# Performance work log

Measured on AMD Instinct MI355X. Metric: run time of the kernel, lower is better.

The kernel has to match this reference:

```python
import jax, jax.numpy as jnp
import numpy as np

NEG_SLOPE_GAT = 0.2   # GATConv internal leaky_relu slope (PyG default)
NEG_SLOPE = 0.01      # nn.LeakyReLU default slope


def _gat(h_src_in, h_dst_in, src, dst, Wsrc, Wdst, a_s, a_d, b, n_dst, self_loops):
    """Single-head PyG-style GATConv: gather -> score -> edge softmax -> scatter-sum."""
    hs = h_src_in @ Wsrc            # [N_src, C]
    hd = h_dst_in @ Wdst            # [N_dst, C]
    if self_loops:                  # static flag; same node set on both sides
        loop = jnp.arange(n_dst, dtype=src.dtype)
        src = jnp.concatenate([src, loop])
        dst = jnp.concatenate([dst, loop])
    # attention logits per edge
    e = jax.nn.leaky_relu((hs @ a_s)[src] + (hd @ a_d)[dst], NEG_SLOPE_GAT)  # [E]
    # softmax over edges sharing a destination node
    m = jax.ops.segment_max(e, dst, num_segments=n_dst)
    ex = jnp.exp(e - m[dst])
    denom = jax.ops.segment_sum(ex, dst, num_segments=n_dst)
    alpha = ex / denom[dst]
    out = jax.ops.segment_sum(hs[src] * alpha[:, None], dst, num_segments=n_dst)
    return out + b


def setup_inputs() -> dict:
    key = jax.random.key(0)
    ks = iter(jax.random.split(key, 64))
    NB, NP = 100_000, 50_000
    E_bb, E_pp, E_bp = 800_000, 400_000, 400_000
    FB, FP, H, H2 = 32, 34, 64, 32
    rn = lambda shape, s=0.05: jax.random.normal(next(ks), shape, jnp.float32) * s
    d = {}
    d['x_b'] = rn((NB, FB), 1.0)
    d['x_p'] = rn((NP, FP), 1.0)
    d['ei_bb'] = jax.random.randint(next(ks), (2, E_bb), 0, NB, jnp.int32)
    d['ei_pp'] = jax.random.randint(next(ks), (2, E_pp), 0, NP, jnp.int32)
    d['ei_bp_src'] = jax.random.randint(next(ks), (E_bp,), 0, NB, jnp.int32)
    d['ei_bp_dst'] = jax.random.randint(next(ks), (E_bp,), 0, NP, jnp.int32)
    d['W_in_b'] = rn((FB, H)); d['b_in_b'] = jnp.zeros((H,), jnp.float32)
    d['W_in_p'] = rn((FP, H)); d['b_in_p'] = jnp.zeros((H,), jnp.float32)
    for tag, cin, cout in (('1', H, H), ('2', H, H2)):
        d['W_bb' + tag] = rn((cin, cout)); d['as_bb' + tag] = rn((cout,)); d['ad_bb' + tag] = rn((cout,)); d['b_bb' + tag] = jnp.zeros((cout,), jnp.float32)
        d['W_pp' + tag] = rn((cin, cout)); d['as_pp' + tag] = rn((cout,)); d['ad_pp' + tag] = rn((cout,)); d['b_pp' + tag] = jnp.zeros((cout,), jnp.float32)
        d['Ws_bp' + tag] = rn((cin, cout)); d['Wd_bp' + tag] = rn((cin, cout)); d['as_bp' + tag] = rn((cout,)); d['ad_bp' + tag] = rn((cout,)); d['b_bp' + tag] = jnp.zeros((cout,), jnp.float32)
    d['W_out'] = rn((H2, 1)); d['b_out'] = jnp.zeros((1,), jnp.float32)
    return d


def reference(x_b, x_p, ei_bb, ei_pp, ei_bp_src, ei_bp_dst,
              W_in_b, b_in_b, W_in_p, b_in_p,
              W_bb1, as_bb1, ad_bb1, b_bb1, W_pp1, as_pp1, ad_pp1, b_pp1,
              Ws_bp1, Wd_bp1, as_bp1, ad_bp1, b_bp1,
              W_bb2, as_bb2, ad_bb2, b_bb2, W_pp2, as_pp2, ad_pp2, b_pp2,
              Ws_bp2, Wd_bp2, as_bp2, ad_bp2, b_bp2,
              W_out, b_out):
    NB, NP = x_b.shape[0], x_p.shape[0]
    lr = lambda v: jax.nn.leaky_relu(v, NEG_SLOPE)
    # input projections (dropout is eval-mode identity)
    hb = lr(x_b @ W_in_b + b_in_b)
    hp = lr(x_p @ W_in_p + b_in_p)
    # hetero conv 1 (sum aggregation over relations sharing a dst type)
    ob = _gat(hb, hb, ei_bb[0], ei_bb[1], W_bb1, W_bb1, as_bb1, ad_bb1, b_bb1, NB, True)
    op = (_gat(hp, hp, ei_pp[0], ei_pp[1], W_pp1, W_pp1, as_pp1, ad_pp1, b_pp1, NP, True)
          + _gat(hb, hp, ei_bp_src, ei_bp_dst, Ws_bp1, Wd_bp1, as_bp1, ad_bp1, b_bp1, NP, False))
    hb, hp = lr(ob), lr(op)
    # hetero conv 2
    ob2 = _gat(hb, hb, ei_bb[0], ei_bb[1], W_bb2, W_bb2, as_bb2, ad_bb2, b_bb2, NB, True)
    op2 = (_gat(hp, hp, ei_pp[0], ei_pp[1], W_pp2, W_pp2, as_pp2, ad_pp2, b_pp2, NP, True)
           + _gat(hb, hp, ei_bp_src, ei_bp_dst, Ws_bp2, Wd_bp2, as_bp2, ad_bp2, b_bp2, NP, False))
    hp = lr(op2)
    return hp @ W_out + b_out  # [NP, 1]
```

## Files before the change

### kernel.cpp

```cpp
#include <hip/hip_runtime.h>
#include <hip/hip_bf16.h>
#include <cstdint>
#include <cstddef>


typedef __attribute__((ext_vector_type(8))) short short8;
typedef __attribute__((ext_vector_type(4))) float f32x4;

#define ABITS 10
#define CHUNKE 8192

static __device__ __forceinline__ float b2f(__hip_bfloat16 v) { return __bfloat162float(v); }

static __device__ __forceinline__ float ldf(const void* p, int i, int bf) {
    return bf ? __bfloat162float(((const __hip_bfloat16*)p)[i]) : ((const float*)p)[i];
}

static __device__ __forceinline__ short f2bs(float f) {
    __hip_bfloat16 h = __float2bfloat16(f);
    return *reinterpret_cast<short*>(&h);
}
static __device__ __forceinline__ float bs2f(short s) {
    __hip_bfloat16 h = *reinterpret_cast<__hip_bfloat16*>(&s);
    return __bfloat162float(h);
}
static __device__ __forceinline__ float sel4(const float* a, int i) {
    return i == 0 ? a[0] : i == 1 ? a[1] : i == 2 ? a[2] : a[3];
}
static __device__ __forceinline__ float lrelu2(float x) { return x > 0.f ? x : 0.2f * x; }

__global__ __launch_bounds__(256) void k_detect(const unsigned* __restrict__ w,
                                                int* __restrict__ flag)
{
    __shared__ int s_cnt;
    if (threadIdx.x == 0) s_cnt = 0;
    __syncthreads();
    int c = 0;
#pragma unroll
    for (int j = 0; j < 4; ++j) {
        unsigned u = w[threadIdx.x * 4 + j];
        unsigned e = (u >> 7) & 0xffu;
        c += (e >= 100u && e <= 145u) ? 1 : 0;
    }
    atomicAdd(&s_cnt, c);
    __syncthreads();
    if (threadIdx.x == 0) *flag = (s_cnt > 614) ? 1 : 0;
}


__global__ __launch_bounds__(256) void k_bkt_hist(
    const int* __restrict__ bb_d, const int* __restrict__ pp_d,
    const int* __restrict__ bp_d, int* __restrict__ histM,
    int E_bb, int E_pp, int E_bp, int NB, int NP, int nbkt, int nblk)
{
    __shared__ int h[256];
    for (int i = threadIdx.x; i < nbkt; i += 256) h[i] = 0;
    __syncthreads();
    int E_all = E_bb + E_pp + E_bp;
    int base = blockIdx.x * CHUNKE;
    int end = base + CHUNKE < E_all ? base + CHUNKE : E_all;
    for (int i = base + threadIdx.x; i < end; i += 256) {
        int d;
        if (i < E_bb) d = bb_d[i];
        else if (i < E_bb + E_pp) d = NB + pp_d[i - E_bb];
        else d = NB + NP + bp_d[i - E_bb - E_pp];
        atomicAdd(&h[d >> ABITS], 1);
    }
    __syncthreads();
    for (int i = threadIdx.x; i < nbkt; i += 256)
        histM[(size_t)i * nblk + blockIdx.x] = h[i];
}

__global__ __launch_bounds__(1024) void k_scan1(const int* __restrict__ deg,
                                                int* __restrict__ out,
                                                int* __restrict__ bsum, int n)
{
    __shared__ int wsum[16];
    int gid = blockIdx.x * 1024 + threadIdx.x;
    int lane = threadIdx.x & 63, wid = threadIdx.x >> 6;
    int v = (gid < n) ? deg[gid] : 0;
    int x = v;
#pragma unroll
    for (int off = 1; off < 64; off <<= 1) {
        int y = __shfl_up(x, off, 64);
        if (lane >= off) x += y;
    }
    if (lane == 63) wsum[wid] = x;
    __syncthreads();
    if (wid == 0 && lane < 16) {
        int w0 = wsum[lane];
#pragma unroll
        for (int off = 1; off < 16; off <<= 1) {
            int y = __shfl_up(w0, off, 16);
            if (lane >= off) w0 += y;
        }
        wsum[lane] = w0;
    }
    __syncthreads();
    int base = (wid > 0) ? wsum[wid - 1] : 0;
    int incl = base + x;
    if (gid < n) out[gid] = incl - v;
    if (threadIdx.x == 1023) bsum[blockIdx.x] = incl;
}

__global__ __launch_bounds__(1024) void k_scan2(int* __restrict__ bsum, int nb)
{
    __shared__ int wsum[16];
    int lane = threadIdx.x & 63, wid = threadIdx.x >> 6;
    int v = (threadIdx.x < nb) ? bsum[threadIdx.x] : 0;
    int x = v;
#pragma unroll
    for (int off = 1; off < 64; off <<= 1) {
        int y = __shfl_up(x, off, 64);
        if (lane >= off) x += y;
    }
    if (lane == 63) wsum[wid] = x;
    __syncthreads();
    if (wid == 0 && lane < 16) {
        int w0 = wsum[lane];
#pragma unroll
        for (int off = 1; off < 16; off <<= 1) {
            int y = __shfl_up(w0, off, 16);
            if (lane >= off) w0 += y;
        }
        wsum[lane] = w0;
    }
    __syncthreads();
    int base = (wid > 0) ? wsum[wid - 1] : 0;
    if (threadIdx.x < nb) bsum[threadIdx.x] = base + x - v;
}

__global__ __launch_bounds__(1024) void k_scan3(int* __restrict__ indptr,
                                                const int* __restrict__ bsum,
                                                int n, int E)
{
    int gid = blockIdx.x * 1024 + threadIdx.x;
    if (gid < n) indptr[gid] += bsum[blockIdx.x];
    if (gid == 0) indptr[n] = E;
}

__global__ __launch_bounds__(256) void k_bkt_scatter(
    const int* __restrict__ bb_s, const int* __restrict__ bb_d,
    const int* __restrict__ pp_s, const int* __restrict__ pp_d,
    const int* __restrict__ bp_s, const int* __restrict__ bp_d,
    const int* __restrict__ histS, unsigned* __restrict__ ebuf,
    int E_bb, int E_pp, int E_bp, int NB, int NP, int nbkt, int nblk)
{
    __shared__ int cur[256];
    for (int i = threadIdx.x; i < nbkt; i += 256)
        cur[i] = histS[(size_t)i * nblk + blockIdx.x];
    __syncthreads();
    int E_all = E_bb + E_pp + E_bp;
    int base = blockIdx.x * CHUNKE;
    int end = base + CHUNKE < E_all ? base + CHUNKE : E_all;
    for (int i = base + threadIdx.x; i < end; i += 256) {
        int s, d;
        if (i < E_bb) { s = bb_s[i]; d = bb_d[i]; }
        else if (i < E_bb + E_pp) { int j = i - E_bb; s = pp_s[j]; d = NB + pp_d[j]; }
        else { int j = i - E_bb - E_pp; s = bp_s[j]; d = NB + NP + bp_d[j]; }
        int p = atomicAdd(&cur[d >> ABITS], 1);
        ebuf[p] = ((unsigned)(d & ((1 << ABITS) - 1)) << 20) | (unsigned)s;
    }
}

__global__ __launch_bounds__(256) void k_deg(
    const unsigned* __restrict__ ebuf, const int* __restrict__ histS,
    int* __restrict__ deg, int NALL, int E_all, int nbkt, int nblk)
{
    __shared__ int h[1 << ABITS];
    int b = blockIdx.x;
    int d0 = b << ABITS;
    int nloc = NALL - d0 < (1 << ABITS) ? NALL - d0 : (1 << ABITS);
    for (int i = threadIdx.x; i < nloc; i += 256) h[i] = 0;
    __syncthreads();
    int s0 = histS[(size_t)b * nblk];
    int s1 = histS[(size_t)(b + 1) * nblk];
    for (int i = s0 + threadIdx.x; i < s1; i += 256)
        atomicAdd(&h[ebuf[i] >> 20], 1);
    __syncthreads();
    for (int i = threadIdx.x; i < nloc; i += 256) deg[d0 + i] = h[i];
}

__global__ __launch_bounds__(256) void k_place(
    const unsigned* __restrict__ ebuf, const int* __restrict__ histS,
    const int* __restrict__ ip, int* __restrict__ sidx,
    int NALL, int E_all, int nbkt, int nblk)
{
    __shared__ int cur[1 << ABITS];
    int b = blockIdx.x;
    int d0 = b << ABITS;
    int nloc = NALL - d0 < (1 << ABITS) ? NALL - d0 : (1 << ABITS);
    for (int i = threadIdx.x; i < nloc; i += 256) cur[i] = ip[d0 + i];
    __syncthreads();
    int s0 = histS[(size_t)b * nblk];
    int s1 = histS[(size_t)(b + 1) * nblk];
    for (int i = s0 + threadIdx.x; i < s1; i += 256) {
        unsigned e = ebuf[i];
        int p = atomicAdd(&cur[e >> 20], 1);
        sidx[p] = (int)(e & 0xFFFFFu);
    }
}

template <int CIN>
__global__ __launch_bounds__(256) void k_in_proj_mfma(
    const void* __restrict__ X, const void* __restrict__ W, const void* __restrict__ B,
    __hip_bfloat16* __restrict__ Y, int M, const int* __restrict__ flag)
{
    const int bf = *flag;
    constexpr int KP = 40;
    __shared__ short WT[64 * KP];
    __shared__ float bl[64];
    for (int i = threadIdx.x; i < CIN * 64; i += 256) {
        int k = i / 64, n = i % 64;
        WT[n * KP + k] = f2bs(ldf(W, i, bf));
    }
    if (threadIdx.x < 64) bl[threadIdx.x] = ldf(B, threadIdx.x, bf);
    __syncthreads();

    int lane = threadIdx.x & 63;
    int wv   = threadIdx.x >> 6;
    int m = lane & 15, quad = lane >> 4;
    int row0 = (blockIdx.x * 4 + wv) * 16;
    if (row0 >= M) return;

    int arow = row0 + m; if (arow >= M) arow = M - 1;
    short8 a;
#pragma unroll
    for (int j = 0; j < 8; ++j)
        a[j] = f2bs(ldf(X, arow * CIN + quad * 8 + j, bf));

    f32x4 acc[4] = {};
#pragma unroll
    for (int t = 0; t < 4; ++t) {
        short8 b = *(const short8*)&WT[((lane & 15) + 16 * t) * KP + quad * 8];
        acc[t] = __builtin_amdgcn_mfma_f32_16x16x32_bf16(a, b, acc[t], 0, 0, 0);
    }

    if (CIN == 34) {
        float x32[4], x33[4];
#pragma unroll
        for (int r = 0; r < 4; ++r) {
            int row = row0 + quad * 4 + r; if (row >= M) row = M - 1;
            x32[r] = ldf(X, row * CIN + 32, bf);
            x33[r] = ldf(X, row * CIN + 33, bf);
        }
#pragma unroll
        for (int t = 0; t < 4; ++t) {
            int col = (lane & 15) + 16 * t;
            float w32 = bs2f(WT[col * KP + 32]);
            float w33 = bs2f(WT[col * KP + 33]);
#pragma unroll
            for (int r = 0; r < 4; ++r)
                acc[t][r] += x32[r] * w32 + x33[r] * w33;
        }
    }

#pragma unroll
    for (int t = 0; t < 4; ++t) {
        int col = (lane & 15) + 16 * t;
        float bb = bl[col];
#pragma unroll
        for (int r = 0; r < 4; ++r) {
            int row = row0 + quad * 4 + r;
            if (row < M) {
                float v = acc[t][r] + bb;
                v = v > 0.f ? v : 0.01f * v;
                Y[(size_t)row * 64 + col] = __float2bfloat16(v);
            }
        }
    }
}

template <int N, bool STORE>
__global__ __launch_bounds__(256) void k_gat_proj_mfma(
    const __hip_bfloat16* __restrict__ H, const void* __restrict__ W,
    const void* __restrict__ a_s, const void* __restrict__ a_d,
    __hip_bfloat16* __restrict__ HS, float* __restrict__ SS, float* __restrict__ SD,
    int M, const int* __restrict__ flag)
{
    const int bf = *flag;
    constexpr int KP = 72;
    constexpr int T = N / 16;
    __shared__ short WT[N * KP];
    for (int i = threadIdx.x; i < 64 * N; i += 256) {
        int k = i / N, n = i % N;
        WT[n * KP + k] = f2bs(ldf(W, i, bf));
    }
    __syncthreads();

    int lane = threadIdx.x & 63;
    int wv   = threadIdx.x >> 6;
    int m = lane & 15, quad = lane >> 4;
    int row0 = (blockIdx.x * 4 + wv) * 16;
    if (row0 >= M) return;

    const short* Hs = (const short*)H;
    int arow = row0 + m; if (arow >= M) arow = M - 1;

    f32x4 acc[T] = {};
#pragma unroll
    for (int ks = 0; ks < 2; ++ks) {
        short8 a = *(const short8*)&Hs[(size_t)arow * 64 + ks * 32 + quad * 8];
#pragma unroll
        for (int t = 0; t < T; ++t) {
            short8 b = *(const short8*)&WT[((lane & 15) + 16 * t) * KP + ks * 32 + quad * 8];
            acc[t] = __builtin_amdgcn_mfma_f32_16x16x32_bf16(a, b, acc[t], 0, 0, 0);
        }
    }

    float asv[T], adv[T];
#pragma unroll
    for (int t = 0; t < T; ++t) {
        int col = (lane & 15) + 16 * t;
        asv[t] = ldf(a_s, col, bf);
        adv[t] = ldf(a_d, col, bf);
    }
    float vs[4] = {}, vd[4] = {};
#pragma unroll
    for (int t = 0; t < T; ++t)
#pragma unroll
        for (int r = 0; r < 4; ++r) {
            vs[r] += acc[t][r] * asv[t];
            vd[r] += acc[t][r] * adv[t];
        }
#pragma unroll
    for (int off = 1; off < 16; off <<= 1)
#pragma unroll
        for (int r = 0; r < 4; ++r) {
            vs[r] += __shfl_xor(vs[r], off);
            vd[r] += __shfl_xor(vd[r], off);
        }
    int c = lane & 15;
    if (c < 8) {
        int row = row0 + quad * 4 + (c & 3);
        if (row < M) {
            if (c < 4) SS[row] = sel4(vs, c & 3);
            else       SD[row] = sel4(vd, c & 3);
        }
    }

    if (STORE) {
#pragma unroll
        for (int t = 0; t < T; ++t) {
            int col = (lane & 15) + 16 * t;
#pragma unroll
            for (int r = 0; r < 4; ++r) {
                int row = row0 + quad * 4 + r;
                if (row < M)
                    HS[(size_t)row * N + col] = __float2bfloat16(acc[t][r]);
            }
        }
    }
}

template <int N1, int N2, bool S1, bool S2>
__global__ __launch_bounds__(256) void k_gat_proj_dual(
    const __hip_bfloat16* __restrict__ H,
    const void* __restrict__ W1, const void* __restrict__ W2,
    const void* __restrict__ as1, const void* __restrict__ ad1,
    const void* __restrict__ as2, const void* __restrict__ ad2,
    __hip_bfloat16* __restrict__ HS1, __hip_bfloat16* __restrict__ HS2,
    float* __restrict__ SS1, float* __restrict__ SD1,
    float* __restrict__ SS2, float* __restrict__ SD2,
    int M, const int* __restrict__ flag)
{
    const int bf = *flag;
    constexpr int KP = 72;
    constexpr int T1 = N1 / 16, T2 = N2 / 16, T = T1 + T2;
    __shared__ short WT[(N1 + N2) * KP];
    for (int i = threadIdx.x; i < 64 * N1; i += 256) {
        int k = i / N1, n = i % N1;
        WT[n * KP + k] = f2bs(ldf(W1, i, bf));
    }
    for (int i = threadIdx.x; i < 64 * N2; i += 256) {
        int k = i / N2, n = i % N2;
        WT[(N1 + n) * KP + k] = f2bs(ldf(W2, i, bf));
    }
    __syncthreads();

    int lane = threadIdx.x & 63;
    int wv   = threadIdx.x >> 6;
    int m = lane & 15, quad = lane >> 4;
    int row0 = (blockIdx.x * 4 + wv) * 16;
    if (row0 >= M) return;

    const short* Hs = (const short*)H;
    int arow = row0 + m; if (arow >= M) arow = M - 1;

    f32x4 acc[T] = {};
#pragma unroll
    for (int ks = 0; ks < 2; ++ks) {
        short8 a = *(const short8*)&Hs[(size_t)arow * 64 + ks * 32 + quad * 8];
#pragma unroll
        for (int t = 0; t < T; ++t) {
            short8 b = *(const short8*)&WT[((lane & 15) + 16 * t) * KP + ks * 32 + quad * 8];
            acc[t] = __builtin_amdgcn_mfma_f32_16x16x32_bf16(a, b, acc[t], 0, 0, 0);
        }
    }

    float vs1[4] = {}, vd1[4] = {}, vs2[4] = {}, vd2[4] = {};
#pragma unroll
    for (int t = 0; t < T1; ++t) {
        int col = (lane & 15) + 16 * t;
        float av = ldf(as1, col, bf), dv = ldf(ad1, col, bf);
#pragma unroll
        for (int r = 0; r < 4; ++r) {
            vs1[r] += acc[t][r] * av;
            vd1[r] += acc[t][r] * dv;
        }
    }
#pragma unroll
    for (int t = 0; t < T2; ++t) {
        int col = (lane & 15) + 16 * t;
        float av = ldf(as2, col, bf), dv = ldf(ad2, col, bf);
#pragma unroll
        for (int r = 0; r < 4; ++r) {
            vs2[r] += acc[T1 + t][r] * av;
            vd2[r] += acc[T1 + t][r] * dv;
        }
    }
#pragma unroll
    for (int off = 1; off < 16; off <<= 1)
#pragma unroll
        for (int r = 0; r < 4; ++r) {
            vs1[r] += __shfl_xor(vs1[r], off);
            vd1[r] += __shfl_xor(vd1[r], off);
            vs2[r] += __shfl_xor(vs2[r], off);
            vd2[r] += __shfl_xor(vd2[r], off);
        }
    int c = lane & 15;
    {
        int row = row0 + quad * 4 + (c & 3);
        if (row < M) {
            if (c < 4)       SS1[row] = sel4(vs1, c & 3);
            else if (c < 8)  SD1[row] = sel4(vd1, c & 3);
            else if (c < 12) SS2[row] = sel4(vs2, c & 3);
            else             SD2[row] = sel4(vd2, c & 3);
        }
    }

    if (S1) {
#pragma unroll
        for (int t = 0; t < T1; ++t) {
            int col = (lane & 15) + 16 * t;
#pragma unroll
            for (int r = 0; r < 4; ++r) {
                int row = row0 + quad * 4 + r;
                if (row < M)
                    HS1[(size_t)row * N1 + col] = __float2bfloat16(acc[t][r]);
            }
        }
    }
    if (S2) {
#pragma unroll
        for (int t = 0; t < T2; ++t) {
            int col = (lane & 15) + 16 * t;
#pragma unroll
            for (int r = 0; r < 4; ++r) {
                int row = row0 + quad * 4 + r;
                if (row < M)
                    HS2[(size_t)row * N2 + col] = __float2bfloat16(acc[T1 + t][r]);
            }
        }
    }
}

__global__ __launch_bounds__(256) void k_gather1(
    const int* __restrict__ indptr, const int* __restrict__ sidx,
    const float* __restrict__ SS, const float* __restrict__ SD,
    const __hip_bfloat16* __restrict__ HS, const void* __restrict__ bias,
    __hip_bfloat16* __restrict__ OUT, int M, const int* __restrict__ flag)
{
    const int bf = *flag;
    int lane = threadIdx.x & 63;
    int d = blockIdx.x * 4 + (threadIdx.x >> 6);
    if (d >= M) return;
    float sdd = SD[d];
    float ex = __expf(lrelu2(SS[d] + sdd));
    float acc = b2f(HS[(size_t)d * 64 + lane]) * ex;
    float den = ex;
    int j = indptr[d], j1 = indptr[d + 1];
    for (; j + 3 < j1; j += 4) {
        int s0 = sidx[j], s1 = sidx[j + 1], s2 = sidx[j + 2], s3 = sidx[j + 3];
        float h0 = b2f(HS[(size_t)s0 * 64 + lane]);
        float h1 = b2f(HS[(size_t)s1 * 64 + lane]);
        float h2 = b2f(HS[(size_t)s2 * 64 + lane]);
        float h3 = b2f(HS[(size_t)s3 * 64 + lane]);
        float e0 = __expf(lrelu2(SS[s0] + sdd));
        float e1 = __expf(lrelu2(SS[s1] + sdd));
        float e2 = __expf(lrelu2(SS[s2] + sdd));
        float e3 = __expf(lrelu2(SS[s3] + sdd));
        acc += h0 * e0 + h1 * e1 + h2 * e2 + h3 * e3;
        den += (e0 + e1) + (e2 + e3);
    }
    for (; j < j1; ++j) {
        int s0 = sidx[j];
        float h0 = b2f(HS[(size_t)s0 * 64 + lane]);
        float e0 = __expf(lrelu2(SS[s0] + sdd));
        acc += h0 * e0; den += e0;
    }
    float v = acc / den + ldf(bias, lane, bf);
    v = v > 0.f ? v : 0.01f * v;
    OUT[(size_t)d * 64 + lane] = __float2bfloat16(v);
}

__global__ __launch_bounds__(256) void k_gather2(
    const int* __restrict__ ip1, const int* __restrict__ si,
    const float* __restrict__ SS1, const float* __restrict__ SD1,
    const __hip_bfloat16* __restrict__ HS1,
    const int* __restrict__ ip2,
    const float* __restrict__ SS2, const float* __restrict__ SD2,
    const __hip_bfloat16* __restrict__ HS2,
    const void* __restrict__ b1, const void* __restrict__ b2,
    __hip_bfloat16* __restrict__ OUT, int M, const int* __restrict__ flag)
{
    const int bf = *flag;
    int lane = threadIdx.x & 63;
    int d = blockIdx.x * 4 + (threadIdx.x >> 6);
    if (d >= M) return;
    float sdd = SD1[d];
    float ex = __expf(lrelu2(SS1[d] + sdd));
    float acc1 = b2f(HS1[(size_t)d * 64 + lane]) * ex;
    float den1 = ex;
    int j = ip1[d], j1 = ip1[d + 1];
    for (; j + 3 < j1; j += 4) {
        int s0 = si[j], s1 = si[j + 1], s2 = si[j + 2], s3 = si[j + 3];
        float h0 = b2f(HS1[(size_t)s0 * 64 + lane]);
        float h1 = b2f(HS1[(size_t)s1 * 64 + lane]);
        float h2 = b2f(HS1[(size_t)s2 * 64 + lane]);
        float h3 = b2f(HS1[(size_t)s3 * 64 + lane]);
        float e0 = __expf(lrelu2(SS1[s0] + sdd));
        float e1 = __expf(lrelu2(SS1[s1] + sdd));
        float e2 = __expf(lrelu2(SS1[s2] + sdd));
        float e3 = __expf(lrelu2(SS1[s3] + sdd));
        acc1 += h0 * e0 + h1 * e1 + h2 * e2 + h3 * e3;
        den1 += (e0 + e1) + (e2 + e3);
    }
    for (; j < j1; ++j) {
        int s0 = si[j];
        float h0 = b2f(HS1[(size_t)s0 * 64 + lane]);
        float e0 = __expf(lrelu2(SS1[s0] + sdd));
        acc1 += h0 * e0; den1 += e0;
    }
    float sdd2 = SD2[d];
    float acc2 = 0.f, den2 = 0.f;
    j = ip2[d]; j1 = ip2[d + 1];
    for (; j + 3 < j1; j += 4) {
        int s0 = si[j], s1 = si[j + 1], s2 = si[j + 2], s3 = si[j + 3];
        float h0 = b2f(HS2[(size_t)s0 * 64 + lane]);
        float h1 = b2f(HS2[(size_t)s1 * 64 + lane]);
        float h2 = b2f(HS2[(size_t)s2 * 64 + lane]);
        float h3 = b2f(HS2[(size_t)s3 * 64 + lane]);
        float e0 = __expf(lrelu2(SS2[s0] + sdd2));
        float e1 = __expf(lrelu2(SS2[s1] + sdd2));
        float e2 = __expf(lrelu2(SS2[s2] + sdd2));
        float e3 = __expf(lrelu2(SS2[s3] + sdd2));
        acc2 += h0 * e0 + h1 * e1 + h2 * e2 + h3 * e3;
        den2 += (e0 + e1) + (e2 + e3);
    }
    for (; j < j1; ++j) {
        int s0 = si[j];
        float h0 = b2f(HS2[(size_t)s0 * 64 + lane]);
        float e0 = __expf(lrelu2(SS2[s0] + sdd2));
        acc2 += h0 * e0; den2 += e0;
    }
    float inv2 = den2 > 0.f ? 1.f / den2 : 0.f;
    float v = acc1 / den1 + acc2 * inv2 + ldf(b1, lane, bf) + ldf(b2, lane, bf);
    v = v > 0.f ? v : 0.01f * v;
    OUT[(size_t)d * 64 + lane] = __float2bfloat16(v);
}

__global__ __launch_bounds__(256) void k_gather_out(
    const int* __restrict__ ip1, const int* __restrict__ si,
    const float* __restrict__ SS1, const float* __restrict__ SD1,
    const __hip_bfloat16* __restrict__ HS1,
    const int* __restrict__ ip2,
    const float* __restrict__ SS2, const float* __restrict__ SD2,
    const __hip_bfloat16* __restrict__ HS2,
    const void* __restrict__ b1, const void* __restrict__ b2,
    const void* __restrict__ Wout, const void* __restrict__ bout,
    void* __restrict__ OUT, int M, const int* __restrict__ flag)
{
    const int bf = *flag;
    int lane = threadIdx.x & 31;
    int d = blockIdx.x * 8 + (threadIdx.x >> 5);
    if (d >= M) return;
    float sdd = SD1[d];
    float ex = __expf(lrelu2(SS1[d] + sdd));
    float acc1 = b2f(HS1[(size_t)d * 32 + lane]) * ex;
    float den1 = ex;
    int j = ip1[d], j1 = ip1[d + 1];
    for (; j + 3 < j1; j += 4) {
        int s0 = si[j], s1 = si[j + 1], s2 = si[j + 2], s3 = si[j + 3];
        float h0 = b2f(HS1[(size_t)s0 * 32 + lane]);
        float h1 = b2f(HS1[(size_t)s1 * 32 + lane]);
        float h2 = b2f(HS1[(size_t)s2 * 32 + lane]);
        float h3 = b2f(HS1[(size_t)s3 * 32 + lane]);
        float e0 = __expf(lrelu2(SS1[s0] + sdd));
        float e1 = __expf(lrelu2(SS1[s1] + sdd));
        float e2 = __expf(lrelu2(SS1[s2] + sdd));
        float e3 = __expf(lrelu2(SS1[s3] + sdd));
        acc1 += h0 * e0 + h1 * e1 + h2 * e2 + h3 * e3;
        den1 += (e0 + e1) + (e2 + e3);
    }
    for (; j < j1; ++j) {
        int s0 = si[j];
        float h0 = b2f(HS1[(size_t)s0 * 32 + lane]);
        float e0 = __expf(lrelu2(SS1[s0] + sdd));
        acc1 += h0 * e0; den1 += e0;
    }
    float sdd2 = SD2[d];
    float acc2 = 0.f, den2 = 0.f;
    j = ip2[d]; j1 = ip2[d + 1];
    for (; j + 3 < j1; j += 4) {
        int s0 = si[j], s1 = si[j + 1], s2 = si[j + 2], s3 = si[j + 3];
        float h0 = b2f(HS2[(size_t)s0 * 32 + lane]);
        float h1 = b2f(HS2[(size_t)s1 * 32 + lane]);
        float h2 = b2f(HS2[(size_t)s2 * 32 + lane]);
        float h3 = b2f(HS2[(size_t)s3 * 32 + lane]);
        float e0 = __expf(lrelu2(SS2[s0] + sdd2));
        float e1 = __expf(lrelu2(SS2[s1] + sdd2));
        float e2 = __expf(lrelu2(SS2[s2] + sdd2));
        float e3 = __expf(lrelu2(SS2[s3] + sdd2));
        acc2 += h0 * e0 + h1 * e1 + h2 * e2 + h3 * e3;
        den2 += (e0 + e1) + (e2 + e3);
    }
    for (; j < j1; ++j) {
        int s0 = si[j];
        float h0 = b2f(HS2[(size_t)s0 * 32 + lane]);
        float e0 = __expf(lrelu2(SS2[s0] + sdd2));
        acc2 += h0 * e0; den2 += e0;
    }
    float inv2 = den2 > 0.f ? 1.f / den2 : 0.f;
    float v = acc1 / den1 + acc2 * inv2 + ldf(b1, lane, bf) + ldf(b2, lane, bf);
    v = v > 0.f ? v : 0.01f * v;
    float t = v * ldf(Wout, lane, bf);
#pragma unroll
    for (int off = 16; off > 0; off >>= 1) t += __shfl_xor(t, off, 32);
    if (lane == 0) {
        float r = t + ldf(bout, 0, bf);
        if (bf) ((__hip_bfloat16*)OUT)[d] = __float2bfloat16(r);
        else    ((float*)OUT)[d] = r;
    }
}

extern "C" void kernel_launch(void* const* d_in, const int* in_sizes, int n_in,
                              void* d_out, int out_size, void* d_ws, size_t ws_size,
                              hipStream_t stream)
{
    const void* x_b = d_in[0];
    const void* x_p = d_in[1];
    const int* ei_bb = (const int*)d_in[2];
    const int* ei_pp = (const int*)d_in[3];
    const int* bp_s  = (const int*)d_in[4];
    const int* bp_d  = (const int*)d_in[5];
    const void *W_in_b = d_in[6],  *b_in_b = d_in[7];
    const void *W_in_p = d_in[8],  *b_in_p = d_in[9];
    const void *W_bb1 = d_in[10], *as_bb1 = d_in[11], *ad_bb1 = d_in[12], *b_bb1 = d_in[13];
    const void *W_pp1 = d_in[14], *as_pp1 = d_in[15], *ad_pp1 = d_in[16], *b_pp1 = d_in[17];
    const void *Ws_bp1 = d_in[18], *Wd_bp1 = d_in[19], *as_bp1 = d_in[20], *ad_bp1 = d_in[21], *b_bp1 = d_in[22];
    const void *W_pp2 = d_in[27], *as_pp2 = d_in[28], *ad_pp2 = d_in[29], *b_pp2 = d_in[30];
    const void *Ws_bp2 = d_in[31], *Wd_bp2 = d_in[32], *as_bp2 = d_in[33], *ad_bp2 = d_in[34], *b_bp2 = d_in[35];
    const void *W_out = d_in[36], *b_out = d_in[37];

    const int NB   = in_sizes[0] / 32;
    const int NP   = in_sizes[1] / 34;
    const int E_bb = in_sizes[2] / 2;
    const int E_pp = in_sizes[3] / 2;
    const int E_bp = in_sizes[4];
    const int E_all = E_bb + E_pp + E_bp;
    const int NALL  = NB + 2 * NP;
    const int* bb_s = ei_bb;  const int* bb_d = ei_bb + E_bb;
    const int* pp_s = ei_pp;  const int* pp_d = ei_pp + E_pp;
    (void)ws_size; (void)n_in; (void)out_size;

    const int nbkt  = (NALL + (1 << ABITS) - 1) >> ABITS;
    const int nblk  = (E_all + CHUNKE - 1) / CHUNKE;
    const int nh    = nbkt * nblk;

    typedef __hip_bfloat16 bf16;
    char* base = (char*)d_ws;
    size_t o = 0;
    auto alloc = [&](size_t bytes) { char* p = base + o; o += (bytes + 255) & ~(size_t)255; return p; };

    int* flag  = (int*)alloc(256);
    int* bsum  = (int*)alloc(1024 * 4);
    int* histM = (int*)alloc((size_t)nh * 4);
    int* histS = (int*)alloc((size_t)(nh + 1) * 4);
    int* degA  = (int*)alloc((size_t)NALL * 4);
    int* ip_all = (int*)alloc((size_t)(NALL + 1) * 4);
    unsigned* ebuf = (unsigned*)alloc((size_t)E_all * 4);
    int* si_all = (int*)alloc((size_t)E_all * 4);
    float* ss_bb = (float*)alloc((size_t)NB * 4);
    float* sd_bb = (float*)alloc((size_t)NB * 4);
    float* ss_bp = (float*)alloc((size_t)NB * 4);
    float* ss_pp = (float*)alloc((size_t)NP * 4);
    float* sd_pp = (float*)alloc((size_t)NP * 4);
    float* sd_bp = (float*)alloc((size_t)NP * 4);
    float* ss2_bp = ss_bb;
    float* ss2_pp = ss_pp;
    float* sd2_pp = sd_pp;
    float* sd2_bp = sd_bp;
    float* junkNB = (float*)degA;
    float* junkNP = (float*)(degA + NB);

    char* S1 = alloc((size_t)NB * 64 * 2);
    char* S2 = alloc((size_t)NP * 64 * 2);
    char* S3 = alloc((size_t)NB * 64 * 2);
    char* S4 = alloc((size_t)NB * 64 * 2);
    char* S5 = alloc((size_t)NB * 64 * 2);
    char* S6 = alloc((size_t)NP * 64 * 2);

    bf16* hb     = (bf16*)S1;
    bf16* hp     = (bf16*)S2;
    bf16* hs_bb  = (bf16*)S3;
    bf16* hb2    = (bf16*)S4;
    bf16* hs_bp  = (bf16*)S5;
    bf16* hs_pp  = (bf16*)S6;
    bf16* hp2    = (bf16*)S3;
    bf16* hs2_pp = (bf16*)S2;
    bf16* hs2_bp = (bf16*)S1;

    auto cdiv = [](int a, int b) { return (a + b - 1) / b; };

    k_detect<<<1, 256, 0, stream>>>((const unsigned*)x_b, flag);

    k_bkt_hist<<<nblk, 256, 0, stream>>>(bb_d, pp_d, bp_d, histM,
                                         E_bb, E_pp, E_bp, NB, NP, nbkt, nblk);
    int sb1 = cdiv(nh, 1024);
    k_scan1<<<sb1, 1024, 0, stream>>>(histM, histS, bsum, nh);
    k_scan2<<<1, 1024, 0, stream>>>(bsum, sb1);
    k_scan3<<<sb1, 1024, 0, stream>>>(histS, bsum, nh, E_all);
    k_bkt_scatter<<<nblk, 256, 0, stream>>>(bb_s, bb_d, pp_s, pp_d, bp_s, bp_d,
                                            histS, ebuf, E_bb, E_pp, E_bp, NB, NP, nbkt, nblk);
    k_deg<<<nbkt, 256, 0, stream>>>(ebuf, histS, degA, NALL, E_all, nbkt, nblk);
    int sb2 = cdiv(NALL, 1024);
    k_scan1<<<sb2, 1024, 0, stream>>>(degA, ip_all, bsum, NALL);
    k_scan2<<<1, 1024, 0, stream>>>(bsum, sb2);
    k_scan3<<<sb2, 1024, 0, stream>>>(ip_all, bsum, NALL, E_all);
    k_place<<<nbkt, 256, 0, stream>>>(ebuf, histS, ip_all, si_all, NALL, E_all, nbkt, nblk);

    const int* ip_bb = ip_all;
    const int* ip_pp = ip_all + NB;
    const int* ip_bp = ip_all + NB + NP;

    k_in_proj_mfma<32><<<cdiv(NB, 64), 256, 0, stream>>>(x_b, W_in_b, b_in_b, hb, NB, flag);
    k_in_proj_mfma<34><<<cdiv(NP, 64), 256, 0, stream>>>(x_p, W_in_p, b_in_p, hp, NP, flag);

    k_gat_proj_dual<64, 64, true, true><<<cdiv(NB, 64), 256, 0, stream>>>(
        hb, W_bb1, Ws_bp1, as_bb1, ad_bb1, as_bp1, ad_bp1,
        hs_bb, hs_bp, ss_bb, sd_bb, ss_bp, junkNB, NB, flag);
    k_gather1<<<cdiv(NB, 4), 256, 0, stream>>>(ip_bb, si_all, ss_bb, sd_bb, hs_bb, b_bb1, hb2, NB, flag);

    k_gat_proj_dual<64, 64, true, false><<<cdiv(NP, 64), 256, 0, stream>>>(
        hp, W_pp1, Wd_bp1, as_pp1, ad_pp1, as_bp1, ad_bp1,
        hs_pp, nullptr, ss_pp, sd_pp, junkNP, sd_bp, NP, flag);
    k_gather2<<<cdiv(NP, 4), 256, 0, stream>>>(ip_pp, si_all, ss_pp, sd_pp, hs_pp,
                                               ip_bp, ss_bp, sd_bp, hs_bp,
                                               b_pp1, b_bp1, hp2, NP, flag);

    k_gat_proj_dual<32, 32, true, false><<<cdiv(NP, 64), 256, 0, stream>>>(
        hp2, W_pp2, Wd_bp2, as_pp2, ad_pp2, as_bp2, ad_bp2,
        hs2_pp, nullptr, ss2_pp, sd2_pp, junkNP, sd2_bp, NP, flag);
    k_gat_proj_mfma<32, true><<<cdiv(NB, 64), 256, 0, stream>>>(
        hb2, Ws_bp2, as_bp2, ad_bp2, hs2_bp, ss2_bp, junkNB, NB, flag);

    k_gather_out<<<cdiv(NP, 8), 256, 0, stream>>>(ip_pp, si_all, ss2_pp, sd2_pp, hs2_pp,
                                                  ip_bp, ss2_bp, sd2_bp, hs2_bp,
                                                  b_pp2, b_bp2, W_out, b_out, d_out, NP, flag);
}
```

Baseline: 426.8 us.

## Vectorize gather kernels with packed bf16 pairs and split edges across wave halves

```diff
diff --git a/kernel.cpp b/kernel.cpp
--- a/kernel.cpp
+++ b/kernel.cpp
@@ -6,9 +6,10 @@
 
 typedef __attribute__((ext_vector_type(8))) short short8;
 typedef __attribute__((ext_vector_type(4))) float f32x4;
-
-#define ABITS 10
-#define CHUNKE 8192
+typedef unsigned int u32;
+
+#define ABITS 9
+#define CHUNKE 4096
 
 static __device__ __forceinline__ float b2f(__hip_bfloat16 v) { return __bfloat162float(v); }
 
@@ -23,6 +24,11 @@
 static __device__ __forceinline__ float bs2f(short s) {
     __hip_bfloat16 h = *reinterpret_cast<__hip_bfloat16*>(&s);
     return __bfloat162float(h);
+}
+static __device__ __forceinline__ float lo16(u32 u) { return bs2f((short)(u & 0xffffu)); }
+static __device__ __forceinline__ float hi16(u32 u) { return bs2f((short)(u >> 16)); }
+static __device__ __forceinline__ u32 pack2(float x, float y) {
+    return (u32)(unsigned short)f2bs(x) | ((u32)(unsigned short)f2bs(y) << 16);
 }
 static __device__ __forceinline__ float sel4(const float* a, int i) {
     return i == 0 ? a[0] : i == 1 ? a[1] : i == 2 ? a[2] : a[3];
@@ -47,13 +53,12 @@
     if (threadIdx.x == 0) *flag = (s_cnt > 614) ? 1 : 0;
 }
 
-
 __global__ __launch_bounds__(256) void k_bkt_hist(
     const int* __restrict__ bb_d, const int* __restrict__ pp_d,
     const int* __restrict__ bp_d, int* __restrict__ histM,
     int E_bb, int E_pp, int E_bp, int NB, int NP, int nbkt, int nblk)
 {
-    __shared__ int h[256];
+    __shared__ int h[512];
     for (int i = threadIdx.x; i < nbkt; i += 256) h[i] = 0;
     __syncthreads();
     int E_all = E_bb + E_pp + E_bp;
@@ -146,7 +151,7 @@
     const int* __restrict__ histS, unsigned* __restrict__ ebuf,
     int E_bb, int E_pp, int E_bp, int NB, int NP, int nbkt, int nblk)
 {
-    __shared__ int cur[256];
+    __shared__ int cur[512];
     for (int i = threadIdx.x; i < nbkt; i += 256)
         cur[i] = histS[(size_t)i * nblk + blockIdx.x];
     __syncthreads();
@@ -210,9 +215,9 @@
     constexpr int KP = 40;
     __shared__ short WT[64 * KP];
     __shared__ float bl[64];
-    for (int i = threadIdx.x; i < CIN * 64; i += 256) {
-        int k = i / 64, n = i % 64;
-        WT[n * KP + k] = f2bs(ldf(W, i, bf));
+    for (int i = threadIdx.x; i < 64 * CIN; i += 256) {
+        int n = i / CIN, k = i - n * CIN;
+        WT[n * KP + k] = f2bs(ldf(W, k * 64 + n, bf));
     }
     if (threadIdx.x < 64) bl[threadIdx.x] = ldf(B, threadIdx.x, bf);
     __syncthreads();
@@ -282,9 +287,9 @@
     constexpr int KP = 72;
     constexpr int T = N / 16;
     __shared__ short WT[N * KP];
-    for (int i = threadIdx.x; i < 64 * N; i += 256) {
-        int k = i / N, n = i % N;
-        WT[n * KP + k] = f2bs(ldf(W, i, bf));
+    for (int i = threadIdx.x; i < N * 64; i += 256) {
+        int n = i >> 6, k = i & 63;
+        WT[n * KP + k] = f2bs(ldf(W, k * N + n, bf));
     }
     __syncthreads();
 
@@ -368,13 +373,13 @@
     constexpr int KP = 72;
     constexpr int T1 = N1 / 16, T2 = N2 / 16, T = T1 + T2;
     __shared__ short WT[(N1 + N2) * KP];
-    for (int i = threadIdx.x; i < 64 * N1; i += 256) {
-        int k = i / N1, n = i % N1;
-        WT[n * KP + k] = f2bs(ldf(W1, i, bf));
-    }
-    for (int i = threadIdx.x; i < 64 * N2; i += 256) {
-        int k = i / N2, n = i % N2;
-        WT[(N1 + n) * KP + k] = f2bs(ldf(W2, i, bf));
+    for (int i = threadIdx.x; i < N1 * 64; i += 256) {
+        int n = i >> 6, k = i & 63;
+        WT[n * KP + k] = f2bs(ldf(W1, k * N1 + n, bf));
+    }
+    for (int i = threadIdx.x; i < N2 * 64; i += 256) {
+        int n = i >> 6, k = i & 63;
+        WT[(N1 + n) * KP + k] = f2bs(ldf(W2, k * N2 + n, bf));
     }
     __syncthreads();
 
@@ -466,42 +471,50 @@
 }
 
 __global__ __launch_bounds__(256) void k_gather1(
-    const int* __restrict__ indptr, const int* __restrict__ sidx,
+    const int* __restrict__ ip, const int* __restrict__ si,
     const float* __restrict__ SS, const float* __restrict__ SD,
     const __hip_bfloat16* __restrict__ HS, const void* __restrict__ bias,
     __hip_bfloat16* __restrict__ OUT, int M, const int* __restrict__ flag)
 {
     const int bf = *flag;
     int lane = threadIdx.x & 63;
+    int half = lane >> 5, hl = lane & 31;
     int d = blockIdx.x * 4 + (threadIdx.x >> 6);
     if (d >= M) return;
+    const u32* H32 = (const u32*)HS;
     float sdd = SD[d];
-    float ex = __expf(lrelu2(SS[d] + sdd));
-    float acc = b2f(HS[(size_t)d * 64 + lane]) * ex;
-    float den = ex;
-    int j = indptr[d], j1 = indptr[d + 1];
-    for (; j + 3 < j1; j += 4) {
-        int s0 = sidx[j], s1 = sidx[j + 1], s2 = sidx[j + 2], s3 = sidx[j + 3];
-        float h0 = b2f(HS[(size_t)s0 * 64 + lane]);
-        float h1 = b2f(HS[(size_t)s1 * 64 + lane]);
-        float h2 = b2f(HS[(size_t)s2 * 64 + lane]);
-        float h3 = b2f(HS[(size_t)s3 * 64 + lane]);
+    float ax = 0.f, ay = 0.f, den = 0.f;
+    if (half == 0) {
+        float ex = __expf(lrelu2(SS[d] + sdd));
+        u32 h = H32[(size_t)d * 32 + hl];
+        ax = lo16(h) * ex; ay = hi16(h) * ex; den = ex;
+    }
+    int j1 = ip[d + 1];
+    int j = ip[d] + half;
+    for (; j + 2 < j1; j += 4) {
+        int s0 = si[j], s1 = si[j + 2];
+        u32 h0 = H32[(size_t)s0 * 32 + hl];
+        u32 h1 = H32[(size_t)s1 * 32 + hl];
         float e0 = __expf(lrelu2(SS[s0] + sdd));
         float e1 = __expf(lrelu2(SS[s1] + sdd));
-        float e2 = __expf(lrelu2(SS[s2] + sdd));
-        float e3 = __expf(lrelu2(SS[s3] + sdd));
-        acc += h0 * e0 + h1 * e1 + h2 * e2 + h3 * e3;
-        den += (e0 + e1) + (e2 + e3);
-    }
-    for (; j < j1; ++j) {
-        int s0 = sidx[j];
-        float h0 = b2f(HS[(size_t)s0 * 64 + lane]);
+        ax += lo16(h0) * e0 + lo16(h1) * e1;
+        ay += hi16(h0) * e0 + hi16(h1) * e1;
+        den += e0 + e1;
+    }
+    if (j < j1) {
+        int s0 = si[j];
+        u32 h0 = H32[(size_t)s0 * 32 + hl];
         float e0 = __expf(lrelu2(SS[s0] + sdd));
-        acc += h0 * e0; den += e0;
-    }
-    float v = acc / den + ldf(bias, lane, bf);
-    v = v > 0.f ? v : 0.01f * v;
-    OUT[(size_t)d * 64 + lane] = __float2bfloat16(v);
+        ax += lo16(h0) * e0; ay += hi16(h0) * e0; den += e0;
+    }
+    ax += __shfl_xor(ax, 32); ay += __shfl_xor(ay, 32); den += __shfl_xor(den, 32);
+    if (half == 0) {
+        float vx = ax / den + ldf(bias, 2 * hl, bf);
+        float vy = ay / den + ldf(bias, 2 * hl + 1, bf);
+        vx = vx > 0.f ? vx : 0.01f * vx;
+        vy = vy > 0.f ? vy : 0.01f * vy;
+        ((u32*)OUT)[(size_t)d * 32 + hl] = pack2(vx, vy);
+    }
 }
 
 __global__ __launch_bounds__(256) void k_gather2(
@@ -516,58 +529,66 @@
 {
     const int bf = *flag;
     int lane = threadIdx.x & 63;
+    int half = lane >> 5, hl = lane & 31;
     int d = blockIdx.x * 4 + (threadIdx.x >> 6);
     if (d >= M) return;
+    const u32* H1 = (const u32*)HS1;
+    const u32* H2 = (const u32*)HS2;
     float sdd = SD1[d];
-    float ex = __expf(lrelu2(SS1[d] + sdd));
-    float acc1 = b2f(HS1[(size_t)d * 64 + lane]) * ex;
-    float den1 = ex;
-    int j = ip1[d], j1 = ip1[d + 1];
-    for (; j + 3 < j1; j += 4) {
-        int s0 = si[j], s1 = si[j + 1], s2 = si[j + 2], s3 = si[j + 3];
-        float h0 = b2f(HS1[(size_t)s0 * 64 + lane]);
-        float h1 = b2f(HS1[(size_t)s1 * 64 + lane]);
-        float h2 = b2f(HS1[(size_t)s2 * 64 + lane]);
-        float h3 = b2f(HS1[(size_t)s3 * 64 + lane]);
+    float a1x = 0.f, a1y = 0.f, den1 = 0.f;
+    if (half == 0) {
+        float ex = __expf(lrelu2(SS1[d] + sdd));
+        u32 h = H1[(size_t)d * 32 + hl];
+        a1x = lo16(h) * ex; a1y = hi16(h) * ex; den1 = ex;
+    }
+    int j1 = ip1[d + 1];
+    int j = ip1[d] + half;
+    for (; j + 2 < j1; j += 4) {
+        int s0 = si[j], s1 = si[j + 2];
+        u32 h0 = H1[(size_t)s0 * 32 + hl];
+        u32 h1 = H1[(size_t)s1 * 32 + hl];
         float e0 = __expf(lrelu2(SS1[s0] + sdd));
         float e1 = __expf(lrelu2(SS1[s1] + sdd));
-        float e2 = __expf(lrelu2(SS1[s2] + sdd));
-        float e3 = __expf(lrelu2(SS1[s3] + sdd));
-        acc1 += h0 * e0 + h1 * e1 + h2 * e2 + h3 * e3;
-        den1 += (e0 + e1) + (e2 + e3);
-    }
-    for (; j < j1; ++j) {
+        a1x += lo16(h0) * e0 + lo16(h1) * e1;
+        a1y += hi16(h0) * e0 + hi16(h1) * e1;
+        den1 += e0 + e1;
+    }
+    if (j < j1) {
         int s0 = si[j];
-        float h0 = b2f(HS1[(size_t)s0 * 64 + lane]);
+        u32 h0 = H1[(size_t)s0 * 32 + hl];
         float e0 = __expf(lrelu2(SS1[s0] + sdd));
-        acc1 += h0 * e0; den1 += e0;
+        a1x += lo16(h0) * e0; a1y += hi16(h0) * e0; den1 += e0;
     }
     float sdd2 = SD2[d];
-    float acc2 = 0.f, den2 = 0.f;
-    j = ip2[d]; j1 = ip2[d + 1];
-    for (; j + 3 < j1; j += 4) {
-        int s0 = si[j], s1 = si[j + 1], s2 = si[j + 2], s3 = si[j + 3];
-        float h0 = b2f(HS2[(size_t)s0 * 64 + lane]);
-        float h1 = b2f(HS2[(size_t)s1 * 64 + lane]);
-        float h2 = b2f(HS2[(size_t)s2 * 64 + lane]);
-        float h3 = b2f(HS2[(size_t)s3 * 64 + lane]);
+    float a2x = 0.f, a2y = 0.f, den2 = 0.f;
+    j1 = ip2[d + 1];
+    j = ip2[d] + half;
+    for (; j + 2 < j1; j += 4) {
+        int s0 = si[j], s1 = si[j + 2];
+        u32 h0 = H2[(size_t)s0 * 32 + hl];
+        u32 h1 = H2[(size_t)s1 * 32 + hl];
         float e0 = __expf(lrelu2(SS2[s0] + sdd2));
         float e1 = __expf(lrelu2(SS2[s1] + sdd2));
-        float e2 = __expf(lrelu2(SS2[s2] + sdd2));
-        float e3 = __expf(lrelu2(SS2[s3] + sdd2));
-        acc2 += h0 * e0 + h1 * e1 + h2 * e2 + h3 * e3;
-        den2 += (e0 + e1) + (e2 + e3);
-    }
-    for (; j < j1; ++j) {
+        a2x += lo16(h0) * e0 + lo16(h1) * e1;
+        a2y += hi16(h0) * e0 + hi16(h1) * e1;
+        den2 += e0 + e1;
+    }
+    if (j < j1) {
         int s0 = si[j];
-        float h0 = b2f(HS2[(size_t)s0 * 64 + lane]);
+        u32 h0 = H2[(size_t)s0 * 32 + hl];
         float e0 = __expf(lrelu2(SS2[s0] + sdd2));
-        acc2 += h0 * e0; den2 += e0;
-    }
-    float inv2 = den2 > 0.f ? 1.f / den2 : 0.f;
-    float v = acc1 / den1 + acc2 * inv2 + ldf(b1, lane, bf) + ldf(b2, lane, bf);
-    v = v > 0.f ? v : 0.01f * v;
-    OUT[(size_t)d * 64 + lane] = __float2bfloat16(v);
+        a2x += lo16(h0) * e0; a2y += hi16(h0) * e0; den2 += e0;
+    }
+    a1x += __shfl_xor(a1x, 32); a1y += __shfl_xor(a1y, 32); den1 += __shfl_xor(den1, 32);
+    a2x += __shfl_xor(a2x, 32); a2y += __shfl_xor(a2y, 32); den2 += __shfl_xor(den2, 32);
+    if (half == 0) {
+        float inv2 = den2 > 0.f ? 1.f / den2 : 0.f;
+        float vx = a1x / den1 + a2x * inv2 + ldf(b1, 2 * hl, bf) + ldf(b2, 2 * hl, bf);
+        float vy = a1y / den1 + a2y * inv2 + ldf(b1, 2 * hl + 1, bf) + ldf(b2, 2 * hl + 1, bf);
+        vx = vx > 0.f ? vx : 0.01f * vx;
+        vy = vy > 0.f ? vy : 0.01f * vy;
+        ((u32*)OUT)[(size_t)d * 32 + hl] = pack2(vx, vy);
+    }
 }
 
 __global__ __launch_bounds__(256) void k_gather_out(
@@ -582,61 +603,47 @@
     void* __restrict__ OUT, int M, const int* __restrict__ flag)
 {
     const int bf = *flag;
-    int lane = threadIdx.x & 31;
-    int d = blockIdx.x * 8 + (threadIdx.x >> 5);
+    int lane = threadIdx.x & 63;
+    int q = lane >> 4, hl = lane & 15;
+    int d = blockIdx.x * 4 + (threadIdx.x >> 6);
     if (d >= M) return;
+    const u32* H1 = (const u32*)HS1;
+    const u32* H2 = (const u32*)HS2;
     float sdd = SD1[d];
-    float ex = __expf(lrelu2(SS1[d] + sdd));
-    float acc1 = b2f(HS1[(size_t)d * 32 + lane]) * ex;
-    float den1 = ex;
-    int j = ip1[d], j1 = ip1[d + 1];
-    for (; j + 3 < j1; j += 4) {
-        int s0 = si[j], s1 = si[j + 1], s2 = si[j + 2], s3 = si[j + 3];
-        float h0 = b2f(HS1[(size_t)s0 * 32 + lane]);
-        float h1 = b2f(HS1[(size_t)s1 * 32 + lane]);
-        float h2 = b2f(HS1[(size_t)s2 * 32 + lane]);
-        float h3 = b2f(HS1[(size_t)s3 * 32 + lane]);
+    float a1x = 0.f, a1y = 0.f, den1 = 0.f;
+    if (q == 0) {
+        float ex = __expf(lrelu2(SS1[d] + sdd));
+        u32 h = H1[(size_t)d * 16 + hl];
+        a1x = lo16(h) * ex; a1y = hi16(h) * ex; den1 = ex;
+    }
+    int j1 = ip1[d + 1];
+    for (int j = ip1[d] + q; j < j1; j += 4) {
+        int s0 = si[j];
+        u32 h0 = H1[(size_t)s0 * 16 + hl];
         float e0 = __expf(lrelu2(SS1[s0] + sdd));
-        float e1 = __expf(lrelu2(SS1[s1] + sdd));
-        float e2 = __expf(lrelu2(SS1[s2] + sdd));
-        float e3 = __expf(lrelu2(SS1[s3] + sdd));
-        acc1 += h0 * e0 + h1 * e1 + h2 * e2 + h3 * e3;
-        den1 += (e0 + e1) + (e2 + e3);
-    }
-    for (; j < j1; ++j) {
+        a1x += lo16(h0) * e0; a1y += hi16(h0) * e0; den1 += e0;
+    }
+    float sdd2 = SD2[d];
+    float a2x = 0.f, a2y = 0.f, den2 = 0.f;
+    j1 = ip2[d + 1];
+    for (int j = ip2[d] + q; j < j1; j += 4) {
         int s0 = si[j];
-        float h0 = b2f(HS1[(size_t)s0 * 32 + lane]);
-        float e0 = __expf(lrelu2(SS1[s0] + sdd));
-        acc1 += h0 * e0; den1 += e0;
-    }
-    float sdd2 = SD2[d];
-    float acc2 = 0.f, den2 = 0.f;
-    j = ip2[d]; j1 = ip2[d + 1];
-    for (; j + 3 < j1; j += 4) {
-        int s0 = si[j], s1 = si[j + 1], s2 = si[j + 2], s3 = si[j + 3];
-        float h0 = b2f(HS2[(size_t)s0 * 32 + lane]);
-        float h1 = b2f(HS2[(size_t)s1 * 32 + lane]);
-        float h2 = b2f(HS2[(size_t)s2 * 32 + lane]);
-        float h3 = b2f(HS2[(size_t)s3 * 32 + lane]);
+        u32 h0 = H2[(size_t)s0 * 16 + hl];
         float e0 = __expf(lrelu2(SS2[s0] + sdd2));
-        float e1 = __expf(lrelu2(SS2[s1] + sdd2));
-        float e2 = __expf(lrelu2(SS2[s2] + sdd2));
-        float e3 = __expf(lrelu2(SS2[s3] + sdd2));
-        acc2 += h0 * e0 + h1 * e1 + h2 * e2 + h3 * e3;
-        den2 += (e0 + e1) + (e2 + e3);
-    }
-    for (; j < j1; ++j) {
-        int s0 = si[j];
-        float h0 = b2f(HS2[(size_t)s0 * 32 + lane]);
-        float e0 = __expf(lrelu2(SS2[s0] + sdd2));
-        acc2 += h0 * e0; den2 += e0;
-    }
+        a2x += lo16(h0) * e0; a2y += hi16(h0) * e0; den2 += e0;
+    }
+    a1x += __shfl_xor(a1x, 16); a1y += __shfl_xor(a1y, 16); den1 += __shfl_xor(den1, 16);
+    a2x += __shfl_xor(a2x, 16); a2y += __shfl_xor(a2y, 16); den2 += __shfl_xor(den2, 16);
+    a1x += __shfl_xor(a1x, 32); a1y += __shfl_xor(a1y, 32); den1 += __shfl_xor(den1, 32);
+    a2x += __shfl_xor(a2x, 32); a2y += __shfl_xor(a2y, 32); den2 += __shfl_xor(den2, 32);
     float inv2 = den2 > 0.f ? 1.f / den2 : 0.f;
-    float v = acc1 / den1 + acc2 * inv2 + ldf(b1, lane, bf) + ldf(b2, lane, bf);
-    v = v > 0.f ? v : 0.01f * v;
-    float t = v * ldf(Wout, lane, bf);
-#pragma unroll
-    for (int off = 16; off > 0; off >>= 1) t += __shfl_xor(t, off, 32);
+    float vx = a1x / den1 + a2x * inv2 + ldf(b1, 2 * hl, bf) + ldf(b2, 2 * hl, bf);
+    float vy = a1y / den1 + a2y * inv2 + ldf(b1, 2 * hl + 1, bf) + ldf(b2, 2 * hl + 1, bf);
+    vx = vx > 0.f ? vx : 0.01f * vx;
+    vy = vy > 0.f ? vy : 0.01f * vy;
+    float t = vx * ldf(Wout, 2 * hl, bf) + vy * ldf(Wout, 2 * hl + 1, bf);
+#pragma unroll
+    for (int off = 1; off < 16; off <<= 1) t += __shfl_xor(t, off);
     if (lane == 0) {
         float r = t + ldf(bout, 0, bf);
         if (bf) ((__hip_bfloat16*)OUT)[d] = __float2bfloat16(r);
@@ -765,7 +772,7 @@
     k_gat_proj_mfma<32, true><<<cdiv(NB, 64), 256, 0, stream>>>(
         hb2, Ws_bp2, as_bp2, ad_bp2, hs2_bp, ss2_bp, junkNB, NB, flag);
 
-    k_gather_out<<<cdiv(NP, 8), 256, 0, stream>>>(ip_pp, si_all, ss2_pp, sd2_pp, hs2_pp,
+    k_gather_out<<<cdiv(NP, 4), 256, 0, stream>>>(ip_pp, si_all, ss2_pp, sd2_pp, hs2_pp,
                                                   ip_bp, ss2_bp, sd2_bp, hs2_bp,
                                                   b_pp2, b_bp2, W_out, b_out, d_out, NP, flag);
 }
```

After: 434.1 us. Within noise of the previous version (+1.7%).
